# Kernel optimization log

Hardware: AMD Instinct MI355X
Metric: run time of the kernel (lower is better)

## Reference

```python
import jax, jax.numpy as jnp
import numpy as np

# constants mirroring init_kwargs
SPATIAL_STRIDE = 4
RADIUS2 = 0.5 ** 2
K = 32


def _fps(xyz, m):
    """Iterative farthest point sampling. xyz: [N,3] -> idx [m] int32 (starts at index 0, like pointnet2)."""
    n = xyz.shape[0]

    def body(i, carry):
        dist, idx = carry
        cur = xyz[idx[i]]                              # [3]
        d = jnp.sum((xyz - cur) ** 2, axis=-1)          # [N]
        dist = jnp.minimum(dist, d)
        idx = idx.at[i + 1].set(jnp.argmax(dist).astype(jnp.int32))
        return dist, idx

    dist0 = jnp.full((n,), 1e10, xyz.dtype)
    idx0 = jnp.zeros((m,), jnp.int32)
    _, idx = jax.lax.fori_loop(0, m - 1, body, (dist0, idx0))
    return idx


def setup_inputs() -> dict:
    key = jax.random.key(0)
    ks = jax.random.split(key, 5)
    B, T, N, C = 4, 8, 2048, 64
    C_IN = 2 * C + 3  # grouped feat2 + anchor feat1 + xyz displacement
    xyzs = jax.random.uniform(ks[0], (B, T, N, 3), dtype=jnp.float32)
    features = jax.random.normal(ks[1], (B, T, N, C), dtype=jnp.float32)
    w1 = jax.random.normal(ks[2], (C_IN, 128), dtype=jnp.float32) / np.sqrt(C_IN)
    w2 = jax.random.normal(ks[3], (128, 128), dtype=jnp.float32) / np.sqrt(128)
    w3 = jax.random.normal(ks[4], (128, 256), dtype=jnp.float32) / np.sqrt(128)
    return {
        "xyzs": xyzs, "features": features,
        "w1": w1, "b1": jnp.zeros((128,), jnp.float32),
        "w2": w2, "b2": jnp.zeros((128,), jnp.float32),
        "w3": w3, "b3": jnp.zeros((256,), jnp.float32),
    }


def reference(xyzs, features, w1, b1, w2, b2, w3, b3):
    B, T, N, _ = xyzs.shape
    M = N // SPATIAL_STRIDE

    # temporal replicate padding [1,1]
    xp = jnp.concatenate([xyzs[:, :1], xyzs, xyzs[:, -1:]], axis=1)        # [B,T+2,N,3]
    fp = jnp.concatenate([features[:, :1], features, features[:, -1:]], axis=1)
    # frames processed: i = 1..T (stride 1); neighbor frame = i+1
    xyz_a, xyz_n = xp[:, 1:T + 1], xp[:, 2:T + 2]                          # [B,T,N,3]
    feat_a, feat_n = fp[:, 1:T + 1], fp[:, 2:T + 2]                        # [B,T,N,C]

    gather = jax.vmap(jax.vmap(lambda a, i: a[i]))  # over (B, T)

    # FPS on each anchor frame
    idx = jax.vmap(jax.vmap(lambda p: _fps(p, M)))(xyz_a)                  # [B,T,M]
    anchor = gather(xyz_a, idx)                                            # [B,T,M,3]
    f1 = gather(feat_a, idx)                                               # [B,T,M,C]

    # knn of anchors into next frame, with ball-query radius clamp
    d = jnp.sum((anchor[:, :, :, None, :] - xyz_n[:, :, None, :, :]) ** 2, axis=-1)  # [B,T,M,N]
    negd, idxk = jax.lax.top_k(-d, K)                                      # [B,T,M,K]
    idxk = jnp.where(-negd <= RADIUS2, idxk, idxk[..., :1])                # duplicate nearest outside radius

    gxyz = gather(xyz_n, idxk)                                             # [B,T,M,K,3]
    gf2 = gather(feat_n, idxk)                                             # [B,T,M,K,C]
    disp = gxyz - anchor[:, :, :, None, :]
    h = jnp.concatenate(
        [gf2, jnp.broadcast_to(f1[:, :, :, None, :], gf2.shape), disp], axis=-1)  # [B,T,M,K,2C+3]

    h = jax.nn.relu(h @ w1 + b1)
    h = jax.nn.relu(h @ w2 + b2)
    h = jax.nn.relu(h @ w3 + b3)
    new_features = jnp.max(h, axis=3)                                      # [B,T,M,256]
    return anchor, new_features
```

## Files before the change

### kernel.cpp

```cpp
#include <hip/hip_runtime.h>

#define BB 4
#define TT 8
#define NN 2048
#define CC 64
#define MM 512
#define KK 32
#define H3DIM 256
#define RAD2 0.25f
#define FINF 3.4e38f

typedef _Float16 f16x8 __attribute__((ext_vector_type(8)));
typedef _Float16 f16x4 __attribute__((ext_vector_type(4)));
typedef float f32x4 __attribute__((ext_vector_type(4)));

template <int CTRL>
__device__ __forceinline__ float dpp_max_step(float x) {
    int xi = __builtin_bit_cast(int, x);
    int yi = __builtin_amdgcn_update_dpp(xi, xi, CTRL, 0xf, 0xf, false);
    return fmaxf(x, __builtin_bit_cast(float, yi));
}
__device__ __forceinline__ float wave_max64(float x) {
    x = dpp_max_step<0x111>(x);
    x = dpp_max_step<0x112>(x);
    x = dpp_max_step<0x114>(x);
    x = dpp_max_step<0x118>(x);
    x = dpp_max_step<0x142>(x);
    x = dpp_max_step<0x143>(x);
    return __builtin_bit_cast(float, __builtin_amdgcn_readlane(__builtin_bit_cast(int, x), 63));
}
template <int CTRL>
__device__ __forceinline__ unsigned long long dpp_minkey_step(unsigned long long k) {
    int lo = (int)(unsigned)k;
    int hi = (int)(unsigned)(k >> 32);
    int slo = __builtin_amdgcn_update_dpp(lo, lo, CTRL, 0xf, 0xf, false);
    int shi = __builtin_amdgcn_update_dpp(hi, hi, CTRL, 0xf, 0xf, false);
    unsigned long long s = ((unsigned long long)(unsigned)shi << 32) | (unsigned)slo;
    return s < k ? s : k;
}
__device__ __forceinline__ unsigned long long wave_minkey(unsigned long long k) {
    k = dpp_minkey_step<0x111>(k);
    k = dpp_minkey_step<0x112>(k);
    k = dpp_minkey_step<0x114>(k);
    k = dpp_minkey_step<0x118>(k);
    k = dpp_minkey_step<0x142>(k);
    k = dpp_minkey_step<0x143>(k);
    int lo = __builtin_amdgcn_readlane((int)(unsigned)k, 63);
    int hi = __builtin_amdgcn_readlane((int)(unsigned)(k >> 32), 63);
    return ((unsigned long long)(unsigned)hi << 32) | (unsigned)lo;
}

#define FPP_LDS 52224

__global__ __launch_bounds__(256) void k_fps_pp(const float* __restrict__ xyzs,
                                                const float* __restrict__ feats,
                                                const float* __restrict__ w1,
                                                int* __restrict__ fps_idx,
                                                _Float16* __restrict__ Pp) {
    extern __shared__ char fsm[];
    int tid = threadIdx.x;

    if (blockIdx.x < BB * TT) {
        float* sx = (float*)fsm;
        float* sy = sx + NN;
        float* sz = sy + NN;
        float* pd = sz + NN;
        int* pi = (int*)(pd + 8);
        int bt = blockIdx.x;
        int lane = tid & 63, w = tid >> 6;
        const float* src = xyzs + (size_t)bt * NN * 3;
        for (int i = tid; i < NN; i += 256) {
            sx[i] = src[i * 3 + 0];
            sy[i] = src[i * 3 + 1];
            sz[i] = src[i * 3 + 2];
        }
        __syncthreads();

        float px[8], py[8], pz[8], dist[8];
#pragma unroll
        for (int j = 0; j < 8; ++j) {
            int p = tid * 8 + j;
            px[j] = sx[p]; py[j] = sy[p]; pz[j] = sz[p];
            dist[j] = 1e10f;
        }

        int cur = 0;
        if (tid == 0) fps_idx[bt * MM + 0] = 0;
        int pbase = tid * 8;

        for (int it = 1; it < MM; ++it) {
            float cx = sx[cur], cy = sy[cur], cz = sz[cur];
            float bestd = -1.0f;
            int bestp = 0;
#pragma unroll
            for (int j = 0; j < 8; ++j) {
                float dx = px[j] - cx, dy = py[j] - cy, dz = pz[j] - cz;
                float d = dx * dx + dy * dy + dz * dz;
                float nd = fminf(dist[j], d);
                dist[j] = nd;
                if (nd > bestd) { bestd = nd; bestp = pbase + j; }
            }
            float wmax = wave_max64(bestd);
            unsigned long long mask = __ballot(bestd == wmax);
            int wl = __ffsll(mask) - 1;
            int wbp = __builtin_amdgcn_readlane(bestp, wl);
            if (lane == 0) { pd[(it & 1) * 4 + w] = wmax; pi[(it & 1) * 4 + w] = wbp; }
            __syncthreads();
            float bd = pd[(it & 1) * 4 + 0];
            int bp = pi[(it & 1) * 4 + 0];
#pragma unroll
            for (int q = 1; q < 4; ++q) {
                float d2 = pd[(it & 1) * 4 + q];
                int p2 = pi[(it & 1) * 4 + q];
                if (d2 > bd) { bd = d2; bp = p2; }
            }
            cur = bp;
            if (tid == 0) fps_idx[bt * MM + it] = cur;
        }
    } else {
        float* sw = (float*)fsm;
        float* sin_ = sw + 68 * 128;
        for (int i = tid; i < 68 * 128; i += 256) {
            int r = i >> 7, c = i & 127;
            float v = 0.f;
            if (r < 64) v = w1[r * 128 + c];
            else if (r < 67) v = w1[(128 + r - 64) * 128 + c];
            sw[i] = v;
        }
        int row0 = (blockIdx.x - BB * TT) * 64;
        int bt = row0 >> 11;
        int b = bt >> 3, t = bt & 7;
        int tn = (t + 1 < TT) ? (t + 1) : (TT - 1);
        size_t nbase = (size_t)(b * TT + tn) * NN + (row0 & (NN - 1));
        const float* fsrc = feats + nbase * CC;
        const float* xsrc = xyzs + nbase * 3;
        for (int i = tid; i < 1024; i += 256) {
            float4 v = ((const float4*)fsrc)[i];
            int r = i >> 4, c = (i & 15) * 4;
            *(float4*)&sin_[r * 68 + c] = v;
        }
        if (tid < 192) {
            int r = tid / 3, c = tid - r * 3;
            sin_[r * 68 + 64 + c] = xsrc[tid];
        }
        if (tid < 64) sin_[tid * 68 + 67] = 0.f;
        __syncthreads();

        int rowg = tid >> 5, colg = tid & 31;
        float4 acc[8];
#pragma unroll
        for (int i = 0; i < 8; ++i) acc[i] = make_float4(0.f, 0.f, 0.f, 0.f);
        for (int k = 0; k < 68; k += 4) {
            float4 a4[8], b4[4];
#pragma unroll
            for (int i = 0; i < 8; ++i) a4[i] = *(const float4*)&sin_[(rowg * 8 + i) * 68 + k];
#pragma unroll
            for (int kk = 0; kk < 4; ++kk) b4[kk] = *(const float4*)&sw[(k + kk) * 128 + colg * 4];
#pragma unroll
            for (int i = 0; i < 8; ++i) {
#pragma unroll
                for (int kk = 0; kk < 4; ++kk) {
                    float av = (kk == 0) ? a4[i].x : (kk == 1) ? a4[i].y : (kk == 2) ? a4[i].z : a4[i].w;
                    acc[i].x += av * b4[kk].x;
                    acc[i].y += av * b4[kk].y;
                    acc[i].z += av * b4[kk].z;
                    acc[i].w += av * b4[kk].w;
                }
            }
        }
#pragma unroll
        for (int i = 0; i < 8; ++i) {
            f16x4 h;
            h[0] = (_Float16)acc[i].x; h[1] = (_Float16)acc[i].y;
            h[2] = (_Float16)acc[i].z; h[3] = (_Float16)acc[i].w;
            *(f16x4*)&Pp[(size_t)(row0 + rowg * 8 + i) * 128 + colg * 4] = h;
        }
    }
}

#define SM_W2 0
#define SM_W3 32768
#define SM_H1 98304
#define SM_H2 114688
#define SM_B2 131072
#define SM_B3 131584
#define SM_IDX 132608
#define SM_TOTAL (132608 + 64 * KK * 4)

__global__ __launch_bounds__(1024)
__attribute__((amdgpu_waves_per_eu(4, 4)))
void k_mlp(const float* __restrict__ xyzs,
           const float* __restrict__ feats,
           const float* __restrict__ w1,
           const float* __restrict__ b1,
           const int* __restrict__ fps_idx,
           const _Float16* __restrict__ Pp,
           float* __restrict__ Qp,
           const float* __restrict__ w2,
           const float* __restrict__ b2,
           const float* __restrict__ w3,
           const float* __restrict__ b3,
           float* __restrict__ out_anchor,
           float* __restrict__ out_feat) {
    extern __shared__ char smem[];
    int tid = threadIdx.x;
    int bid = ((blockIdx.x & 7) << 5) | (blockIdx.x >> 3);
    int* sidx = (int*)(smem + SM_IDX);

    {
        float* qsw = (float*)smem;
        float* qsin = qsw + 68 * 128;
        float* qsb = qsin + 64 * 68;
        for (int i = tid; i < 68 * 128; i += 1024) {
            int r = i >> 7, c = i & 127;
            float v = 0.f;
            if (r < 64) v = w1[(64 + r) * 128 + c];
            else if (r < 67) v = w1[(128 + r - 64) * 128 + c];
            qsw[i] = v;
        }
        if (tid < 128) qsb[tid] = b1[tid];
        int row0 = bid * 64;
        int bt0 = row0 >> 9;
        size_t fbase = (size_t)bt0 * NN;
        {
            int r = tid >> 4, seg = tid & 15;
            int aidx = fps_idx[row0 + r];
            const float4* fr = (const float4*)(feats + (fbase + aidx) * CC);
            float4 v = fr[seg];
            *(float4*)&qsin[r * 68 + seg * 4] = v;
        }
        if (tid < 64) {
            int aidx = fps_idx[row0 + tid];
            const float* xs = xyzs + (fbase + aidx) * 3;
            float x = xs[0], y = xs[1], z = xs[2];
            qsin[tid * 68 + 64] = -x;
            qsin[tid * 68 + 65] = -y;
            qsin[tid * 68 + 66] = -z;
            qsin[tid * 68 + 67] = 0.f;
            out_anchor[(size_t)(row0 + tid) * 3 + 0] = x;
            out_anchor[(size_t)(row0 + tid) * 3 + 1] = y;
            out_anchor[(size_t)(row0 + tid) * 3 + 2] = z;
        }
        __syncthreads();

        int rowg = tid >> 5, colg = tid & 31;
        float4 bias = *(const float4*)&qsb[colg * 4];
        float4 acc[2];
#pragma unroll
        for (int i = 0; i < 2; ++i) acc[i] = bias;
        for (int k = 0; k < 68; k += 4) {
            float4 a4[2], b4[4];
#pragma unroll
            for (int i = 0; i < 2; ++i) a4[i] = *(const float4*)&qsin[(rowg * 2 + i) * 68 + k];
#pragma unroll
            for (int kk = 0; kk < 4; ++kk) b4[kk] = *(const float4*)&qsw[(k + kk) * 128 + colg * 4];
#pragma unroll
            for (int i = 0; i < 2; ++i) {
#pragma unroll
                for (int kk = 0; kk < 4; ++kk) {
                    float av = (kk == 0) ? a4[i].x : (kk == 1) ? a4[i].y : (kk == 2) ? a4[i].z : a4[i].w;
                    acc[i].x += av * b4[kk].x;
                    acc[i].y += av * b4[kk].y;
                    acc[i].z += av * b4[kk].z;
                    acc[i].w += av * b4[kk].w;
                }
            }
        }
#pragma unroll
        for (int i = 0; i < 2; ++i)
            *(float4*)&Qp[(size_t)(bid * 64 + rowg * 2 + i) * 128 + colg * 4] = acc[i];
    }
    __syncthreads();

    {
        float* sx = (float*)smem;
        float* sy = sx + NN;
        float* sz = sy + NN;
        int row0 = bid * 64;
        int bt = row0 >> 9;
        int b = bt >> 3, t = bt & 7;
        int tn = (t + 1 < TT) ? (t + 1) : (TT - 1);
        const float* src = xyzs + ((size_t)(b * TT + tn)) * NN * 3;
        for (int i = tid; i < NN; i += 1024) {
            sx[i] = src[i * 3 + 0];
            sy[i] = src[i * 3 + 1];
            sz[i] = src[i * 3 + 2];
        }
        __syncthreads();

        int wave = tid >> 6, lane = tid & 63;
        for (int a = 0; a < 4; ++a) {
            int la = wave * 4 + a;
            int mrow = row0 + la;
            int aidx = fps_idx[mrow];
            const float* xs = xyzs + ((size_t)bt * NN + aidx) * 3;
            float ax = xs[0], ay = xs[1], az = xs[2];
            float d[32];
#pragma unroll
            for (int j = 0; j < 32; ++j) {
                int p = j * 64 + lane;
                float dx = sx[p] - ax, dy = sy[p] - ay, dz = sz[p] - az;
                d[j] = dx * dx + dy * dy + dz * dz;
            }
            float gd[4];
            int gp[4];
#pragma unroll
            for (int g = 0; g < 4; ++g) {
                gd[g] = d[g * 8];
                gp[g] = (g * 8) * 64 + lane;
#pragma unroll
                for (int jj = 1; jj < 8; ++jj) {
                    float dj = d[g * 8 + jj];
                    if (dj < gd[g]) { gd[g] = dj; gp[g] = (g * 8 + jj) * 64 + lane; }
                }
            }

            int p0 = 0;
            int myidx = 0;
            for (int r = 0; r < KK; ++r) {
                bool u01 = gd[1] < gd[0], u23 = gd[3] < gd[2];
                float da = u01 ? gd[1] : gd[0], db = u23 ? gd[3] : gd[2];
                int pa = u01 ? gp[1] : gp[0], pb = u23 ? gp[3] : gp[2];
                bool uf = db < da;
                float bd = uf ? db : da;
                int bp = uf ? pb : pa;
                unsigned long long key =
                    ((unsigned long long)(unsigned)__builtin_bit_cast(unsigned, bd) << 32) |
                    (unsigned)bp;
                unsigned long long wkey = wave_minkey(key);
                int pstar = (int)(unsigned)wkey;
                float dstar = __builtin_bit_cast(float, (unsigned)(wkey >> 32));
                if (r == 0) { p0 = pstar; myidx = pstar; }
                int outp = (dstar <= RAD2) ? pstar : p0;
                if (lane == r) myidx = outp;
                if (r < KK - 1) {
                    int lanew = pstar & 63;
                    int jw = pstar >> 6;
                    int gsel = jw >> 3;
                    int jl = jw & 7;
                    bool imw = (lane == lanew);
#define KNN_RECOMP(G)                                                         \
                    {                                                         \
                        _Pragma("unroll")                                     \
                        for (int jj = 0; jj < 8; ++jj) {                      \
                            float dj = d[(G) * 8 + jj];                       \
                            dj = (imw && jj == jl) ? FINF : dj;               \
                            d[(G) * 8 + jj] = dj;                             \
                        }                                                     \
                        gd[G] = d[(G) * 8];                                   \
                        gp[G] = ((G) * 8) * 64 + lane;                        \
                        _Pragma("unroll")                                     \
                        for (int jj = 1; jj < 8; ++jj) {                      \
                            float dj = d[(G) * 8 + jj];                       \
                            if (dj < gd[G]) { gd[G] = dj; gp[G] = ((G) * 8 + jj) * 64 + lane; } \
                        }                                                     \
                    }
                    switch (gsel) {
                        case 0: KNN_RECOMP(0); break;
                        case 1: KNN_RECOMP(1); break;
                        case 2: KNN_RECOMP(2); break;
                        default: KNN_RECOMP(3); break;
                    }
#undef KNN_RECOMP
                }
            }
            if (lane < KK) sidx[la * KK + lane] = myidx;
        }
    }
    __syncthreads();

    for (int i = tid; i < 128 * 128; i += 1024) {
        int n = i & 127, kk = i >> 7;
        _Float16 v = (_Float16)w2[kk * 128 + n];
        *(_Float16*)(smem + SM_W2 + n * 256 + ((2 * kk) ^ ((n & 7) << 4))) = v;
    }
    for (int i = tid; i < 256 * 128; i += 1024) {
        int n = i & 255, kk = i >> 8;
        _Float16 v = (_Float16)w3[kk * 256 + n];
        *(_Float16*)(smem + SM_W3 + n * 256 + ((2 * kk) ^ ((n & 7) << 4))) = v;
    }
    if (tid < 128) *(float*)(smem + SM_B2 + tid * 4) = b2[tid];
    if (tid < 256) *(float*)(smem + SM_B3 + tid * 4) = b3[tid];
    __syncthreads();

    int lane = tid & 63;
    int w = tid >> 6;
    int wm = w >> 3, wn = w & 7;
    int l15 = lane & 15, g = lane >> 4;
    int hswz = (l15 & 7) << 4;

    const f32x4 zero4 = {0.f, 0.f, 0.f, 0.f};

    for (int c = 0; c < 32; ++c) {
        int a0 = bid * 64 + c * 2;
        int bt = a0 >> 9;

        {
            int r = tid >> 4, seg = tid & 15;
            int la = c * 2 + (r >> 5);
            int kidx = r & 31;
            int nk = sidx[la * KK + kidx];
            const _Float16* ps = Pp + ((size_t)(bt * NN + nk)) * 128 + seg * 8;
            const float* qs = Qp + (size_t)(bid * 64 + la) * 128 + seg * 8;
            int rowbase = SM_H1 + r * 256;
            int swz = (r & 7) << 4;
            f16x8 pv = *(const f16x8*)ps;
            f32x4 q0 = *(const f32x4*)qs;
            f32x4 q1 = *(const f32x4*)(qs + 4);
            f16x8 hv;
#pragma unroll
            for (int j = 0; j < 4; ++j) hv[j] = (_Float16)fmaxf((float)pv[j] + q0[j], 0.f);
#pragma unroll
            for (int j = 0; j < 4; ++j) hv[4 + j] = (_Float16)fmaxf((float)pv[4 + j] + q1[j], 0.f);
            *(f16x8*)(smem + rowbase + ((seg * 16) ^ swz)) = hv;
        }
        __syncthreads();

        f32x4 acc2[2];
#pragma unroll
        for (int m = 0; m < 2; ++m) acc2[m] = zero4;

#pragma unroll
        for (int ks = 0; ks < 4; ++ks) {
            int kbyte = ks * 64 + g * 16;
            f16x8 af[2], bf;
#pragma unroll
            for (int m = 0; m < 2; ++m) {
                int row = wm * 32 + m * 16 + l15;
                af[m] = *(const f16x8*)(smem + SM_H1 + row * 256 + (kbyte ^ hswz));
            }
            {
                int col = wn * 16 + l15;
                bf = *(const f16x8*)(smem + SM_W2 + col * 256 + (kbyte ^ hswz));
            }
#pragma unroll
            for (int m = 0; m < 2; ++m)
                acc2[m] = __builtin_amdgcn_mfma_f32_16x16x32_f16(af[m], bf, acc2[m], 0, 0, 0);
        }
#pragma unroll
        for (int m = 0; m < 2; ++m) {
            int col = wn * 16 + l15;
            float bb = *(const float*)(smem + SM_B2 + col * 4);
#pragma unroll
            for (int r = 0; r < 4; ++r) {
                int row = wm * 32 + m * 16 + g * 4 + r;
                float v = fmaxf(acc2[m][r] + bb, 0.f);
                *(_Float16*)(smem + SM_H2 + row * 256 + ((2 * col) ^ ((row & 7) << 4))) = (_Float16)v;
            }
        }
        __syncthreads();

        f32x4 acc3[2][2];
#pragma unroll
        for (int m = 0; m < 2; ++m)
#pragma unroll
            for (int n = 0; n < 2; ++n) acc3[m][n] = zero4;

#pragma unroll
        for (int ks = 0; ks < 4; ++ks) {
            int kbyte = ks * 64 + g * 16;
            f16x8 af[2], bf[2];
#pragma unroll
            for (int m = 0; m < 2; ++m) {
                int row = wm * 32 + m * 16 + l15;
                af[m] = *(const f16x8*)(smem + SM_H2 + row * 256 + (kbyte ^ hswz));
            }
#pragma unroll
            for (int n = 0; n < 2; ++n) {
                int col = wn * 32 + n * 16 + l15;
                bf[n] = *(const f16x8*)(smem + SM_W3 + col * 256 + (kbyte ^ hswz));
            }
#pragma unroll
            for (int m = 0; m < 2; ++m)
#pragma unroll
                for (int n = 0; n < 2; ++n)
                    acc3[m][n] = __builtin_amdgcn_mfma_f32_16x16x32_f16(af[m], bf[n], acc3[m][n], 0, 0, 0);
        }
#pragma unroll
        for (int n = 0; n < 2; ++n) {
            int col = wn * 32 + n * 16 + l15;
            float s = acc3[0][n][0];
#pragma unroll
            for (int r = 1; r < 4; ++r) s = fmaxf(s, acc3[0][n][r]);
#pragma unroll
            for (int r = 0; r < 4; ++r) s = fmaxf(s, acc3[1][n][r]);
            s = fmaxf(s, __shfl_xor(s, 16));
            s = fmaxf(s, __shfl_xor(s, 32));
            if (g == 0) {
                float bb = *(const float*)(smem + SM_B3 + col * 4);
                out_feat[(size_t)(a0 + wm) * H3DIM + col] = fmaxf(s + bb, 0.f);
            }
        }
        __syncthreads();
    }
}

extern "C" void kernel_launch(void* const* d_in, const int* in_sizes, int n_in,
                              void* d_out, int out_size, void* d_ws, size_t ws_size,
                              hipStream_t stream) {
    const float* xyzs  = (const float*)d_in[0];
    const float* feats = (const float*)d_in[1];
    const float* w1 = (const float*)d_in[2];
    const float* b1 = (const float*)d_in[3];
    const float* w2 = (const float*)d_in[4];
    const float* b2 = (const float*)d_in[5];
    const float* w3 = (const float*)d_in[6];
    const float* b3 = (const float*)d_in[7];

    float* out_anchor = (float*)d_out;
    float* out_feat = out_anchor + (size_t)BB * TT * MM * 3;

    char* ws = (char*)d_ws;
    int* fps_idx = (int*)ws;
    _Float16* Pp = (_Float16*)(ws + 65536 + 2097152);
    float* Qp = (float*)(ws + 65536 + 2097152 + 16777216);
    if (ws_size < (size_t)(65536 + 2097152 + 16777216) + (size_t)BB * TT * MM * 128 * 4)
        return;

    (void)hipFuncSetAttribute((const void*)k_fps_pp, hipFuncAttributeMaxDynamicSharedMemorySize, FPP_LDS);
    k_fps_pp<<<BB * TT + BB * TT * NN / 64, 256, FPP_LDS, stream>>>(xyzs, feats, w1, fps_idx, Pp);

    (void)hipFuncSetAttribute((const void*)k_mlp, hipFuncAttributeMaxDynamicSharedMemorySize, SM_TOTAL);
    k_mlp<<<256, 1024, SM_TOTAL, stream>>>(xyzs, feats, w1, b1, fps_idx, Pp, Qp,
                                           w2, b2, w3, b3, out_anchor, out_feat);
}
```

Baseline: 515.4 us.

## Recompute kNN distances from LDS instead of holding 32 per-lane registers

The per-lane array of 32 distances is replaced by a 32-bit taken mask. Each time a group's minimum is refreshed, that group's eight distances are recomputed from the shared-memory xyz. The fixed waves_per_eu(4,4) attribute is also removed, letting the compiler choose register allocation. The aim is to cut VGPR pressure and spills, at the cost of extra LDS reads and arithmetic on every selection round.

```diff
diff --git a/kernel.cpp b/kernel.cpp
--- a/kernel.cpp
+++ b/kernel.cpp
@@ -188,7 +188,6 @@
 #define SM_TOTAL (132608 + 64 * KK * 4)
 
 __global__ __launch_bounds__(1024)
-__attribute__((amdgpu_waves_per_eu(4, 4)))
 void k_mlp(const float* __restrict__ xyzs,
            const float* __restrict__ feats,
            const float* __restrict__ w1,
@@ -295,23 +294,18 @@
             int aidx = fps_idx[mrow];
             const float* xs = xyzs + ((size_t)bt * NN + aidx) * 3;
             float ax = xs[0], ay = xs[1], az = xs[2];
-            float d[32];
-#pragma unroll
-            for (int j = 0; j < 32; ++j) {
-                int p = j * 64 + lane;
-                float dx = sx[p] - ax, dy = sy[p] - ay, dz = sz[p] - az;
-                d[j] = dx * dx + dy * dy + dz * dz;
-            }
+            unsigned taken = 0u;
             float gd[4];
             int gp[4];
 #pragma unroll
             for (int g = 0; g < 4; ++g) {
-                gd[g] = d[g * 8];
-                gp[g] = (g * 8) * 64 + lane;
-#pragma unroll
-                for (int jj = 1; jj < 8; ++jj) {
-                    float dj = d[g * 8 + jj];
-                    if (dj < gd[g]) { gd[g] = dj; gp[g] = (g * 8 + jj) * 64 + lane; }
+#pragma unroll
+                for (int jj = 0; jj < 8; ++jj) {
+                    int p = (g * 8 + jj) * 64 + lane;
+                    float dx = sx[p] - ax, dy = sy[p] - ay, dz = sz[p] - az;
+                    float dj = dx * dx + dy * dy + dz * dz;
+                    if (jj == 0) { gd[g] = dj; gp[g] = p; }
+                    else if (dj < gd[g]) { gd[g] = dj; gp[g] = p; }
                 }
             }
 
@@ -337,22 +331,19 @@
                     int lanew = pstar & 63;
                     int jw = pstar >> 6;
                     int gsel = jw >> 3;
-                    int jl = jw & 7;
+                    unsigned wbit = 1u << jw;
                     bool imw = (lane == lanew);
+                    taken |= imw ? wbit : 0u;
 #define KNN_RECOMP(G)                                                         \
                     {                                                         \
                         _Pragma("unroll")                                     \
                         for (int jj = 0; jj < 8; ++jj) {                      \
-                            float dj = d[(G) * 8 + jj];                       \
-                            dj = (imw && jj == jl) ? FINF : dj;               \
-                            d[(G) * 8 + jj] = dj;                             \
-                        }                                                     \
-                        gd[G] = d[(G) * 8];                                   \
-                        gp[G] = ((G) * 8) * 64 + lane;                        \
-                        _Pragma("unroll")                                     \
-                        for (int jj = 1; jj < 8; ++jj) {                      \
-                            float dj = d[(G) * 8 + jj];                       \
-                            if (dj < gd[G]) { gd[G] = dj; gp[G] = ((G) * 8 + jj) * 64 + lane; } \
+                            int p = ((G) * 8 + jj) * 64 + lane;               \
+                            float dx = sx[p] - ax, dy = sy[p] - ay, dz = sz[p] - az; \
+                            float dd = dx * dx + dy * dy + dz * dz;           \
+                            float dj = ((taken >> ((G) * 8 + jj)) & 1u) ? FINF : dd; \
+                            if (jj == 0) { gd[G] = dj; gp[G] = p; }           \
+                            else if (dj < gd[G]) { gd[G] = dj; gp[G] = p; }   \
                         }                                                     \
                     }
                     switch (gsel) {
```

After: 521.1 us. About the same (+1.1%).
